# Kernel tuning notes

Hardware: AMD Instinct MI355X
Metric: run time of the kernel (lower is better)

Reference implementation:

```python
import jax, jax.numpy as jnp
import numpy as np

TREE_DEPTH = 3
CONSTANTS = jnp.array([-1.0, 0.0, 1.0], dtype=jnp.float32)


def setup_inputs() -> dict:
    key = jax.random.key(0)
    ks = jax.random.split(key, 5)
    B, S, D, W, SLOT = 2, 2048, 1024, 4096, 8
    C = SLOT + 3
    hidden = jax.random.normal(ks[0], (B, S, D), dtype=jnp.float32)
    slot_w = jax.random.normal(ks[1], (D, SLOT), dtype=jnp.float32) * (0.5 / np.sqrt(D))
    slot_b = jnp.zeros((SLOT,), dtype=jnp.float32)
    leaf_logits = jax.random.normal(ks[2], (W, 1 << TREE_DEPTH, C), dtype=jnp.float32) * 0.02
    node_params = jnp.array([1.0, 1.0, 0.25, 0.0, 0.0], dtype=jnp.float32)
    out_w = jax.random.normal(ks[3], (W, D), dtype=jnp.float32) * (0.5 / np.sqrt(W))
    out_b = jnp.zeros((D,), dtype=jnp.float32)
    return {"hidden": hidden, "slot_w": slot_w, "slot_b": slot_b,
            "leaf_logits": leaf_logits, "node_params": node_params,
            "out_w": out_w, "out_b": out_b}


def reference(hidden, slot_w, slot_b, leaf_logits, node_params, out_w, out_b):
    B, S, _ = hidden.shape
    # basis: tanh slot projection concatenated with fixed constants -> [B,S,slot+3]
    slots = jnp.tanh(hidden @ slot_w + slot_b)
    consts = jnp.broadcast_to(CONSTANTS.astype(hidden.dtype), (B, S, 3))
    basis = jnp.concatenate((slots, consts), axis=-1)
    # leaf values: softmax-weighted mixture over the tiny basis dim -> [B,S,W,leaf]
    selector = jax.nn.softmax(leaf_logits.astype(hidden.dtype), axis=-1)
    values = jnp.einsum('wlc,bsc->bswl', selector, basis)
    lw, rw, pw, dw, nb = [p.astype(hidden.dtype) for p in node_params]
    for _ in range(TREE_DEPTH):
        left, right = values[..., 0::2], values[..., 1::2]
        values = jnp.tanh(lw * left + rw * right + pw * left * right
                          + dw * (left - right) + nb)
    roots = values[..., 0]  # [B,S,W]
    return roots @ out_w + out_b
```

## Files before the change

kernel.cpp:

```cpp
#include <hip/hip_runtime.h>
#include <stdint.h>

#define BSZ   4096
#define DIM   1024
#define WTR   4096
#define KDIM  4096
#define W8    32768

typedef unsigned short u16;
typedef __attribute__((ext_vector_type(8))) short bhalf8;
typedef __attribute__((ext_vector_type(4))) float floatx4;
typedef __attribute__((ext_vector_type(16))) float floatx16;

__device__ __forceinline__ u16 f2bf(float f) {
    union { float f; uint32_t i; } v; v.f = f;
    uint32_t r = v.i + 0x7fffu + ((v.i >> 16) & 1u);
    return (u16)(r >> 16);
}
__device__ __forceinline__ float fast_tanh(float x) {
    float e = __builtin_amdgcn_exp2f(x * 2.885390081777927f);
    return fmaf(-2.0f, __builtin_amdgcn_rcpf(e + 1.0f), 1.0f);
}
__device__ __forceinline__ void load16(const void* g, void* lds) {
    __builtin_amdgcn_global_load_lds(
        (const __attribute__((address_space(1))) uint32_t*)g,
        (__attribute__((address_space(3))) uint32_t*)lds, 16, 0, 0);
}

#define NB_SEL   128
#define NB_OWT   4096
#define NB_BASIS 256

__global__ __launch_bounds__(256) void k_prep(const float* __restrict__ ll,
                                              u16* __restrict__ selwA,
                                              const float* __restrict__ ow,
                                              u16* __restrict__ owt,
                                              const float* __restrict__ slot_w,
                                              const float* __restrict__ slot_b,
                                              const float* __restrict__ hidden,
                                              u16* __restrict__ basisTB) {
    __shared__ __align__(16) char smem[20608];
    int bid = blockIdx.x, tid = threadIdx.x;
    if (bid < NB_SEL) {
        int row = bid * 256 + tid;
        int w = row >> 3, l = row & 7, q = w & 3;
        int prow = (w >> 2) * 32 + (l & 3) + 8 * (l >> 2) + 16 * (q & 1) + 4 * (q >> 1);
        const float* p = ll + (size_t)row * 11;
        float v[11]; float m = -1e30f;
        #pragma unroll
        for (int c = 0; c < 11; ++c) { v[c] = p[c]; m = fmaxf(m, v[c]); }
        float s = 0.f;
        #pragma unroll
        for (int c = 0; c < 11; ++c) {
            v[c] = __builtin_amdgcn_exp2f((v[c] - m) * 1.4426950408889634f);
            s += v[c];
        }
        float inv = __builtin_amdgcn_rcpf(s);
        union { u16 h[16]; uint4 qq[2]; } o;
        #pragma unroll
        for (int c = 0; c < 8; ++c) o.h[c] = f2bf(v[c] * inv);
        o.h[8] = f2bf((v[10] - v[8]) * inv);
        #pragma unroll
        for (int c = 9; c < 16; ++c) o.h[c] = 0;
        uint4* dst = (uint4*)(selwA + (size_t)prow * 16);
        dst[0] = o.qq[0]; dst[1] = o.qq[1];
    } else if (bid < NB_SEL + NB_OWT) {
        float (*tile)[33] = (float (*)[33])smem;
        int b = bid - NB_SEL;
        int d0 = (b & 31) * 32, w0 = (b >> 5) * 32;
        int tx = tid & 31, ty = tid >> 5;
        #pragma unroll
        for (int i = 0; i < 32; i += 8)
            tile[ty + i][tx] = ow[(size_t)(w0 + ty + i) * DIM + d0 + tx];
        __syncthreads();
        #pragma unroll
        for (int i = 0; i < 32; i += 8)
            owt[(size_t)(d0 + ty + i) * WTR + w0 + tx] = f2bf(tile[tx][ty + i]);
    } else {
        u16*   sw  = (u16*)smem;
        float* smr = (float*)(smem + 16384);
        int b = bid - NB_SEL - NB_OWT;
        int m0 = b * 16;
        for (int i = tid; i < 8 * 1024; i += 256) {
            int d = i & 1023, s = i >> 10;
            sw[s * 1024 + d] = f2bf(slot_w[(size_t)d * 8 + s]);
        }
        __syncthreads();
        int lane = tid & 63, wid = tid >> 6;
        int col = lane & 15, quad = lane >> 4;
        const float* ga = hidden + (size_t)(m0 + col) * DIM + wid * 256 + quad * 8;
        const u16*   gb = sw + (col & 7) * 1024 + wid * 256 + quad * 8;
        bhalf8 zz = {0, 0, 0, 0, 0, 0, 0, 0};
        floatx4 acc = (floatx4){0.f, 0.f, 0.f, 0.f};
        #pragma unroll
        for (int k0 = 0; k0 < 256; k0 += 32) {
            float4 a0 = *(const float4*)(ga + k0);
            float4 a1 = *(const float4*)(ga + k0 + 4);
            bhalf8 bf = *(const bhalf8*)(gb + k0);
            if (col >= 8) bf = zz;
            bhalf8 af;
            af[0] = (short)f2bf(a0.x); af[1] = (short)f2bf(a0.y);
            af[2] = (short)f2bf(a0.z); af[3] = (short)f2bf(a0.w);
            af[4] = (short)f2bf(a1.x); af[5] = (short)f2bf(a1.y);
            af[6] = (short)f2bf(a1.z); af[7] = (short)f2bf(a1.w);
            acc = __builtin_amdgcn_mfma_f32_16x16x32_bf16(af, bf, acc, 0, 0, 0);
        }
        float (*sm3)[16][16] = (float (*)[16][16])smr;
        #pragma unroll
        for (int r = 0; r < 4; ++r) sm3[wid][quad * 4 + r][col] = acc[r];
        __syncthreads();
        int tt = tid >> 4, cc = tid & 15;
        float s = sm3[0][tt][cc] + sm3[1][tt][cc] + sm3[2][tt][cc] + sm3[3][tt][cc];
        u16 val;
        if (cc < 8)       val = f2bf(fast_tanh(s + slot_b[cc]));
        else if (cc == 8) val = (u16)0x3f80;
        else              val = 0;
        basisTB[(size_t)(m0 + tt) * 16 + cc] = val;
    }
}

__device__ __forceinline__ float tree_eval(float v[8], float A1, float A2,
                                           float A3, float A4) {
    #pragma unroll
    for (int lev = 0; lev < 3; ++lev) {
        int n = 4 >> lev;
        #pragma unroll
        for (int i = 0; i < 4; ++i) {
            if (i < n) {
                float L = v[2*i], R = v[2*i+1];
                float u = fmaf(A2, R, A1);
                float w = fmaf(A3, R, A4);
                float y = fmaf(L, u, w);
                float e = __builtin_amdgcn_exp2f(y);
                v[i] = fmaf(-2.0f, __builtin_amdgcn_rcpf(e + 1.0f), 1.0f);
            }
        }
    }
    return v[0];
}

__global__ __launch_bounds__(256, 2) void k_roots(const u16* __restrict__ selwA,
                                                  const u16* __restrict__ basisTB,
                                                  const float* __restrict__ np_,
                                                  u16* __restrict__ roots) {
    __shared__ uint32_t st[2][32 * 33];
    int tid = threadIdx.x, wid = tid >> 6, lane = tid & 63;
    int c = lane & 31, h = lane >> 5;
    int tile0 = blockIdx.x * 16 + wid * 4;
    int wblk  = blockIdx.x * 64;
    int t0b   = blockIdx.y * 512;
    float lw = np_[0], rw = np_[1], pw = np_[2], dw = np_[3], nb = np_[4];
    const float c2 = 2.885390081777927f;
    float A1 = (lw + dw) * c2, A2 = pw * c2, A3 = (rw - dw) * c2, A4 = nb * c2;

    bhalf8 af[4];
    #pragma unroll
    for (int tl = 0; tl < 4; ++tl)
        af[tl] = *(const bhalf8*)(selwA + (size_t)((tile0 + tl) * 32 + c) * 16 + h * 8);

    int tok = tid >> 3, ch = tid & 7;
    for (int it = 0; it < 16; ++it) {
        int t0 = t0b + it * 32;
        uint32_t* buf = st[it & 1];
        bhalf8 bf = *(const bhalf8*)(basisTB + (size_t)(t0 + c) * 16 + h * 8);
        #pragma unroll
        for (int tl = 0; tl < 4; ++tl) {
            floatx16 z = {0.f,0.f,0.f,0.f,0.f,0.f,0.f,0.f,
                          0.f,0.f,0.f,0.f,0.f,0.f,0.f,0.f};
            floatx16 cc = __builtin_amdgcn_mfma_f32_32x32x16_bf16(af[tl], bf, z, 0, 0, 0);
            float vA[8], vB[8];
            #pragma unroll
            for (int l = 0; l < 8; ++l) { vA[l] = cc[l]; vB[l] = cc[8 + l]; }
            float rA = tree_eval(vA, A1, A2, A3, A4);
            float rB = tree_eval(vB, A1, A2, A3, A4);
            buf[c * 33 + wid * 8 + tl * 2 + h] =
                (uint32_t)f2bf(rA) | ((uint32_t)f2bf(rB) << 16);
        }
        __syncthreads();
        uint32_t d0 = buf[tok * 33 + ch * 4];
        uint32_t d1 = buf[tok * 33 + ch * 4 + 1];
        uint32_t d2 = buf[tok * 33 + ch * 4 + 2];
        uint32_t d3 = buf[tok * 33 + ch * 4 + 3];
        uint4 q; q.x = d0; q.y = d1; q.z = d2; q.w = d3;
        *(uint4*)(roots + (size_t)(t0 + tok) * WTR + wblk + ch * 8) = q;
    }
}

__global__ __launch_bounds__(128) void k_gemm(const u16* __restrict__ A,
                                              const u16* __restrict__ Bt,
                                              const float* __restrict__ out_b,
                                              float* __restrict__ C) {
    __shared__ __align__(16) u16 smA[64 * 64];
    __shared__ __align__(16) u16 smB[64 * 64];
    int tid = threadIdx.x;
    int bm = blockIdx.x * 64, bn = blockIdx.y * 64;
    int lane = tid & 63, wid = tid >> 6;
    int wn = wid * 32;

    floatx4 acc[4][2];
    #pragma unroll
    for (int i = 0; i < 4; ++i)
        #pragma unroll
        for (int j = 0; j < 2; ++j) acc[i][j] = (floatx4){0.f, 0.f, 0.f, 0.f};

    int ar = tid >> 3;
    int ak = ((tid & 7) ^ (ar & 7)) * 8;
    const u16* gA = A  + (size_t)(bm + ar) * KDIM + ak;
    const u16* gB = Bt + (size_t)(bn + ar) * KDIM + ak;
    char* ldA = (char*)smA + tid * 16;
    char* ldB = (char*)smB + tid * 16;

    int col = lane & 15, quad = lane >> 4, csw = col & 7;

    for (int k0 = 0; k0 < KDIM; k0 += 64) {
        __syncthreads();
        load16(gA,                       ldA);
        load16(gA + (size_t)16 * KDIM,   ldA + 2048);
        load16(gA + (size_t)32 * KDIM,   ldA + 4096);
        load16(gA + (size_t)48 * KDIM,   ldA + 6144);
        load16(gB,                       ldB);
        load16(gB + (size_t)16 * KDIM,   ldB + 2048);
        load16(gB + (size_t)32 * KDIM,   ldB + 4096);
        load16(gB + (size_t)48 * KDIM,   ldB + 6144);
        gA += 64; gB += 64;
        __syncthreads();

        #pragma unroll
        for (int kk = 0; kk < 2; ++kk) {
            int kc = kk * 4 + quad;
            bhalf8 af[4], bf[2];
            #pragma unroll
            for (int i = 0; i < 4; ++i)
                af[i] = *(const bhalf8*)(smA + ((i * 16 + col) * 8 + (kc ^ csw)) * 8);
            #pragma unroll
            for (int j = 0; j < 2; ++j)
                bf[j] = *(const bhalf8*)(smB + ((wn + j * 16 + col) * 8 + (kc ^ csw)) * 8);
            #pragma unroll
            for (int i = 0; i < 4; ++i)
                #pragma unroll
                for (int j = 0; j < 2; ++j)
                    acc[i][j] = __builtin_amdgcn_mfma_f32_16x16x32_bf16(
                        af[i], bf[j], acc[i][j], 0, 0, 0);
        }
    }

    #pragma unroll
    for (int j = 0; j < 2; ++j) {
        int n = bn + wn + j * 16 + col;
        float bv = out_b[n];
        #pragma unroll
        for (int i = 0; i < 4; ++i) {
            int m0 = bm + i * 16 + quad * 4;
            #pragma unroll
            for (int r = 0; r < 4; ++r)
                C[(size_t)(m0 + r) * DIM + n] = acc[i][j][r] + bv;
        }
    }
}

extern "C" void kernel_launch(void* const* d_in, const int* in_sizes, int n_in,
                              void* d_out, int out_size, void* d_ws, size_t ws_size,
                              hipStream_t stream) {
    const float* hidden      = (const float*)d_in[0];
    const float* slot_w      = (const float*)d_in[1];
    const float* slot_b      = (const float*)d_in[2];
    const float* leaf_logits = (const float*)d_in[3];
    const float* node_params = (const float*)d_in[4];
    const float* out_w       = (const float*)d_in[5];
    const float* out_b       = (const float*)d_in[6];
    float* out = (float*)d_out;

    char* ws = (char*)d_ws;
    u16* selwA   = (u16*)ws;
    u16* basisTB = (u16*)(ws + 1048576);
    u16* outwt   = (u16*)(ws + 1212416);
    u16* roots   = (u16*)(ws + 9601024);

    k_prep <<<NB_SEL + NB_OWT + NB_BASIS, 256, 0, stream>>>(
        leaf_logits, selwA, out_w, outwt, slot_w, slot_b, hidden, basisTB);
    k_roots<<<dim3(64, 8), 256, 0, stream>>>(selwA, basisTB, node_params, roots);
    k_gemm <<<dim3(BSZ / 64, DIM / 64), 128, 0, stream>>>(roots, outwt, out_b, out);
}
```

Before: 182.3 us.

## Move out_w transpose into roots kernel and drop block-wide sync

The out_w transpose/bf16 conversion moves out of the prep kernel and into extra blocks of the roots kernel, so it can run alongside the MFMA/tree work instead of delaying it. The transpose tiles grow from 32x32 to 64x64, which cuts the block count. The roots kernel now stages results per wave in LDS and stores 16-byte chunks per wave without __syncthreads, so waves no longer wait on each other. In exchange the roots stores become narrower per row (32 bytes per token per wave instead of 128 bytes per block), and the change relies on intra-wave LDS ordering with no explicit barrier.

Measured after the change: 171.5 us. 5.9% less time.

```diff
diff --git a/kernel.cpp b/kernel.cpp
--- a/kernel.cpp
+++ b/kernel.cpp
@@ -28,13 +28,12 @@
 }
 
 #define NB_SEL   128
-#define NB_OWT   4096
 #define NB_BASIS 256
+#define NB_ROOTS 512
+#define NB_OWT   1024
 
 __global__ __launch_bounds__(256) void k_prep(const float* __restrict__ ll,
                                               u16* __restrict__ selwA,
-                                              const float* __restrict__ ow,
-                                              u16* __restrict__ owt,
                                               const float* __restrict__ slot_w,
                                               const float* __restrict__ slot_b,
                                               const float* __restrict__ hidden,
@@ -64,22 +63,10 @@
         for (int c = 9; c < 16; ++c) o.h[c] = 0;
         uint4* dst = (uint4*)(selwA + (size_t)prow * 16);
         dst[0] = o.qq[0]; dst[1] = o.qq[1];
-    } else if (bid < NB_SEL + NB_OWT) {
-        float (*tile)[33] = (float (*)[33])smem;
-        int b = bid - NB_SEL;
-        int d0 = (b & 31) * 32, w0 = (b >> 5) * 32;
-        int tx = tid & 31, ty = tid >> 5;
-        #pragma unroll
-        for (int i = 0; i < 32; i += 8)
-            tile[ty + i][tx] = ow[(size_t)(w0 + ty + i) * DIM + d0 + tx];
-        __syncthreads();
-        #pragma unroll
-        for (int i = 0; i < 32; i += 8)
-            owt[(size_t)(d0 + ty + i) * WTR + w0 + tx] = f2bf(tile[tx][ty + i]);
     } else {
         u16*   sw  = (u16*)smem;
         float* smr = (float*)(smem + 16384);
-        int b = bid - NB_SEL - NB_OWT;
+        int b = bid - NB_SEL;
         int m0 = b * 16;
         for (int i = tid; i < 8 * 1024; i += 256) {
             int d = i & 1023, s = i >> 10;
@@ -142,47 +129,60 @@
 __global__ __launch_bounds__(256, 2) void k_roots(const u16* __restrict__ selwA,
                                                   const u16* __restrict__ basisTB,
                                                   const float* __restrict__ np_,
-                                                  u16* __restrict__ roots) {
-    __shared__ uint32_t st[2][32 * 33];
-    int tid = threadIdx.x, wid = tid >> 6, lane = tid & 63;
-    int c = lane & 31, h = lane >> 5;
-    int tile0 = blockIdx.x * 16 + wid * 4;
-    int wblk  = blockIdx.x * 64;
-    int t0b   = blockIdx.y * 512;
-    float lw = np_[0], rw = np_[1], pw = np_[2], dw = np_[3], nb = np_[4];
-    const float c2 = 2.885390081777927f;
-    float A1 = (lw + dw) * c2, A2 = pw * c2, A3 = (rw - dw) * c2, A4 = nb * c2;
-
-    bhalf8 af[4];
-    #pragma unroll
-    for (int tl = 0; tl < 4; ++tl)
-        af[tl] = *(const bhalf8*)(selwA + (size_t)((tile0 + tl) * 32 + c) * 16 + h * 8);
-
-    int tok = tid >> 3, ch = tid & 7;
-    for (int it = 0; it < 16; ++it) {
-        int t0 = t0b + it * 32;
-        uint32_t* buf = st[it & 1];
-        bhalf8 bf = *(const bhalf8*)(basisTB + (size_t)(t0 + c) * 16 + h * 8);
-        #pragma unroll
-        for (int tl = 0; tl < 4; ++tl) {
-            floatx16 z = {0.f,0.f,0.f,0.f,0.f,0.f,0.f,0.f,
-                          0.f,0.f,0.f,0.f,0.f,0.f,0.f,0.f};
-            floatx16 cc = __builtin_amdgcn_mfma_f32_32x32x16_bf16(af[tl], bf, z, 0, 0, 0);
-            float vA[8], vB[8];
-            #pragma unroll
-            for (int l = 0; l < 8; ++l) { vA[l] = cc[l]; vB[l] = cc[8 + l]; }
-            float rA = tree_eval(vA, A1, A2, A3, A4);
-            float rB = tree_eval(vB, A1, A2, A3, A4);
-            buf[c * 33 + wid * 8 + tl * 2 + h] =
-                (uint32_t)f2bf(rA) | ((uint32_t)f2bf(rB) << 16);
-        }
-        __syncthreads();
-        uint32_t d0 = buf[tok * 33 + ch * 4];
-        uint32_t d1 = buf[tok * 33 + ch * 4 + 1];
-        uint32_t d2 = buf[tok * 33 + ch * 4 + 2];
-        uint32_t d3 = buf[tok * 33 + ch * 4 + 3];
-        uint4 q; q.x = d0; q.y = d1; q.z = d2; q.w = d3;
-        *(uint4*)(roots + (size_t)(t0 + tok) * WTR + wblk + ch * 8) = q;
+                                                  u16* __restrict__ roots,
+                                                  const float* __restrict__ ow,
+                                                  u16* __restrict__ owt) {
+    __shared__ __align__(16) char smem[16640];
+    int bid = blockIdx.x, tid = threadIdx.x;
+    if (bid < NB_ROOTS) {
+        uint32_t* st = (uint32_t*)smem + (tid >> 6) * (32 * 12);
+        int wid = tid >> 6, lane = tid & 63;
+        int c = lane & 31, h = lane >> 5;
+        int bx = bid & 63, by = bid >> 6;
+        int tile0 = bx * 16 + wid * 4;
+        int w0w   = bx * 64 + wid * 16;
+        int t0b   = by * 512;
+        float lw = np_[0], rw = np_[1], pw = np_[2], dw = np_[3], nb = np_[4];
+        const float c2 = 2.885390081777927f;
+        float A1 = (lw + dw) * c2, A2 = pw * c2, A3 = (rw - dw) * c2, A4 = nb * c2;
+
+        bhalf8 af[4];
+        #pragma unroll
+        for (int tl = 0; tl < 4; ++tl)
+            af[tl] = *(const bhalf8*)(selwA + (size_t)((tile0 + tl) * 32 + c) * 16 + h * 8);
+
+        int tok = lane >> 1, half = lane & 1;
+        for (int it = 0; it < 16; ++it) {
+            int t0 = t0b + it * 32;
+            bhalf8 bf = *(const bhalf8*)(basisTB + (size_t)(t0 + c) * 16 + h * 8);
+            #pragma unroll
+            for (int tl = 0; tl < 4; ++tl) {
+                floatx16 z = {0.f,0.f,0.f,0.f,0.f,0.f,0.f,0.f,
+                              0.f,0.f,0.f,0.f,0.f,0.f,0.f,0.f};
+                floatx16 cc = __builtin_amdgcn_mfma_f32_32x32x16_bf16(af[tl], bf, z, 0, 0, 0);
+                float vA[8], vB[8];
+                #pragma unroll
+                for (int l = 0; l < 8; ++l) { vA[l] = cc[l]; vB[l] = cc[8 + l]; }
+                float rA = tree_eval(vA, A1, A2, A3, A4);
+                float rB = tree_eval(vB, A1, A2, A3, A4);
+                st[c * 12 + tl * 2 + h] =
+                    (uint32_t)f2bf(rA) | ((uint32_t)f2bf(rB) << 16);
+            }
+            uint4 q = *(const uint4*)(st + tok * 12 + half * 4);
+            *(uint4*)(roots + (size_t)(t0 + tok) * WTR + w0w + half * 8) = q;
+        }
+    } else {
+        float (*tile)[65] = (float (*)[65])smem;
+        int b = bid - NB_ROOTS;
+        int d0 = (b & 15) * 64, w0 = (b >> 4) * 64;
+        int tx = tid & 63, ty = tid >> 6;
+        #pragma unroll
+        for (int i = 0; i < 64; i += 4)
+            tile[ty + i][tx] = ow[(size_t)(w0 + ty + i) * DIM + d0 + tx];
+        __syncthreads();
+        #pragma unroll
+        for (int i = 0; i < 64; i += 4)
+            owt[(size_t)(d0 + ty + i) * WTR + w0 + tx] = f2bf(tile[tx][ty + i]);
     }
 }
 
@@ -276,8 +276,9 @@
     u16* outwt   = (u16*)(ws + 1212416);
     u16* roots   = (u16*)(ws + 9601024);
 
-    k_prep <<<NB_SEL + NB_OWT + NB_BASIS, 256, 0, stream>>>(
-        leaf_logits, selwA, out_w, outwt, slot_w, slot_b, hidden, basisTB);
-    k_roots<<<dim3(64, 8), 256, 0, stream>>>(selwA, basisTB, node_params, roots);
+    k_prep <<<NB_SEL + NB_BASIS, 256, 0, stream>>>(
+        leaf_logits, selwA, slot_w, slot_b, hidden, basisTB);
+    k_roots<<<NB_ROOTS + NB_OWT, 256, 0, stream>>>(
+        selwA, basisTB, node_params, roots, out_w, outwt);
     k_gemm <<<dim3(BSZ / 64, DIM / 64), 128, 0, stream>>>(roots, outwt, out_b, out);
 }
```
